# Kernel tuning notes

Hardware: AMD Instinct MI355X
Metric: run time of the kernel (lower is better)

## Reference

```python
import jax, jax.numpy as jnp
import numpy as np

BATCH, STEP, IN_DIM, HID = 16384, 5, 11, 512


def setup_inputs() -> dict:
    key = jax.random.key(0)
    k1, k2, k3, k4, k5 = jax.random.split(key, 5)
    s = 1.0 / np.sqrt(HID)  # torch LSTMCell init scale (uniform +-1/sqrt(hidden))
    return {
        "time_series": jax.random.normal(k1, (BATCH, STEP, IN_DIM), jnp.float32),
        "W_ih": jax.random.uniform(k2, (4 * HID, IN_DIM), jnp.float32, -s, s),
        "W_hh": jax.random.uniform(k3, (4 * HID, HID), jnp.float32, -s, s),
        "b_ih": jax.random.uniform(k4, (4 * HID,), jnp.float32, -s, s),
        "b_hh": jax.random.uniform(k5, (4 * HID,), jnp.float32, -s, s),
    }


def _lstm_scan(time_series, W_ih, W_hh, b_ih, b_hh):
    B = time_series.shape[0]
    H = W_hh.shape[1]
    # Precompute input projections for all steps in one big GEMM: [B, T, 4H]
    x_proj = jnp.einsum('bti,gi->btg', time_series, W_ih) + b_ih + b_hh

    def cell(carry, xg):
        h, c = carry
        gates = xg + h @ W_hh.T  # [B, 4H]
        i, f, g, o = jnp.split(gates, 4, axis=-1)  # torch gate order i,f,g,o
        i = jax.nn.sigmoid(i)
        f = jax.nn.sigmoid(f)
        g = jnp.tanh(g)
        o = jax.nn.sigmoid(o)
        c_new = f * c + i * g
        h_new = o * jnp.tanh(c_new)
        return (h_new, c_new), None

    h0 = jnp.zeros((B, H), time_series.dtype)
    c0 = jnp.zeros((B, H), time_series.dtype)
    (h, c), _ = jax.lax.scan(cell, (h0, c0), jnp.swapaxes(x_proj, 0, 1))
    return c  # original module returns the final cell state c


def reference(time_series, W_ih, W_hh, b_ih, b_hh):
    return _lstm_scan(time_series, W_ih, W_hh, b_ih, b_hh)
```

## Files before the change

### kernel.cpp

```cpp
#include <hip/hip_runtime.h>
#include <hip/hip_bf16.h>


#define HID   512
#define ROWS  64
#define NTHR  1024
#define HBBYTES 36864
#define HB    (HBBYTES / 2)
#define SMEM_HALFS (2 * HB + 64 * 56 + 1024)
#define SMEM_BYTES (SMEM_HALFS * 2)

#define WT_I8   0
#define WT_F16X 1048576
#define WT_CSC  1179648

#define L2E   1.442695041f
#define L2E2  2.885390082f

typedef _Float16 f16x8 __attribute__((ext_vector_type(8)));
typedef float f32x4 __attribute__((ext_vector_type(4)));
typedef int v4i __attribute__((ext_vector_type(4)));

__global__ __launch_bounds__(256) void pack_w(const float* __restrict__ Wih,
                                              const float* __restrict__ Whh,
                                              const float* __restrict__ bih,
                                              const float* __restrict__ bhh,
                                              char* __restrict__ Wt) {
    const int col  = blockIdx.x * 4 + (threadIdx.x >> 6);
    const int lane = threadIdx.x & 63;
    const int g = col >> 9;
    const int j = (col & 511) >> 4;
    const int c = col & 15;

    const float4* __restrict__ src = (const float4*)(Whh + (size_t)col * 512);
    float4 u0 = src[lane * 2 + 0];
    float4 u1 = src[lane * 2 + 1];
    float w[8] = {u0.x, u0.y, u0.z, u0.w, u1.x, u1.y, u1.z, u1.w};

    float m = 0.0f;
#pragma unroll
    for (int q = 0; q < 8; q++) m = fmaxf(m, fabsf(w[q]));
#pragma unroll
    for (int off = 32; off >= 1; off >>= 1)
        m = fmaxf(m, __shfl_xor(m, off));
    m = fmaxf(m, 1e-12f);
    const float inv = 127.0f / m;

    unsigned lo = 0, hi = 0;
#pragma unroll
    for (int q = 0; q < 4; q++)
        lo |= ((unsigned)((int)rintf(w[q] * inv) & 0xff)) << (8 * q);
#pragma unroll
    for (int q = 0; q < 4; q++)
        hi |= ((unsigned)((int)rintf(w[4 + q] * inv) & 0xff)) << (8 * q);

    const int ks8 = lane >> 3;
    const int p   = (lane >> 1) & 3;
    const int bo  = (lane & 1) * 8;
    size_t addr = ((size_t)(j * 8 + ks8) * 4 + g) * 1024 + (c + 16 * p) * 16 + bo;
    uint2 pk = {lo, hi};
    *(uint2*)(Wt + WT_I8 + addr) = pk;

    if (lane == 0) {
        float* csc = (float*)(Wt + WT_CSC);
        csc[col] = (m / 16129.0f) * ((g == 2) ? L2E2 : L2E);
    }

    if (lane < 4) {
        const float scale = (g == 2) ? L2E2 : L2E;
        _Float16 t[8];
        const int kb = lane * 8;
#pragma unroll
        for (int q = 0; q < 8; q++) {
            int k = kb + q;
            float x;
            if (k < 11)       x = Wih[col * 11 + k];
            else if (k == 11) x = bih[col] + bhh[col];
            else              x = 0.0f;
            t[q] = (_Float16)(x * scale);
        }
        *(f16x8*)(Wt + WT_F16X + ((size_t)j * 4 + g) * 1024
                  + (c + 16 * lane) * 16) = *(const f16x8*)t;
    }
}

template <bool FIRST, bool WRITE_H>
__device__ __forceinline__ void run_step(const char* __restrict__ cur,
                                         char* __restrict__ nxt,
                                         const char* __restrict__ wbase,
                                         const float (&sc)[2][4],
                                         f32x4* __restrict__ cacc,
                                         const int wave, const int lane) {
    const int c  = lane & 15;
    const int kq = lane >> 4;
    const int lane16 = lane * 16;
#pragma unroll
    for (int ji = 0; ji < 2; ji++) {
        const int j  = wave * 2 + ji;
        const int jj = __builtin_amdgcn_readfirstlane(j);

        v4i acc[4][4];
        if (!FIRST) {
#pragma unroll
            for (int rt = 0; rt < 4; rt++)
#pragma unroll
                for (int g = 0; g < 4; g++) {
                    v4i z = {0, 0, 0, 0};
                    acc[rt][g] = z;
                }
            const char* __restrict__ w0 = wbase + (size_t)jj * 32768;
            const char* __restrict__ ac = cur + lane16;
#pragma unroll 1
            for (int ks = 0; ks < 8; ks++) {
                v4i B0 = *(const v4i*)(w0 + lane16 + 0);
                v4i B1 = *(const v4i*)(w0 + lane16 + 1024);
                v4i B2 = *(const v4i*)(w0 + lane16 + 2048);
                v4i B3 = *(const v4i*)(w0 + lane16 + 3072);
#pragma unroll
                for (int rt = 0; rt < 4; rt++) {
                    v4i A = *(const v4i*)(ac + rt * 1024);
                    acc[rt][0] = __builtin_amdgcn_mfma_i32_16x16x64_i8(A, B0, acc[rt][0], 0, 0, 0);
                    acc[rt][1] = __builtin_amdgcn_mfma_i32_16x16x64_i8(A, B1, acc[rt][1], 0, 0, 0);
                    acc[rt][2] = __builtin_amdgcn_mfma_i32_16x16x64_i8(A, B2, acc[rt][2], 0, 0, 0);
                    acc[rt][3] = __builtin_amdgcn_mfma_i32_16x16x64_i8(A, B3, acc[rt][3], 0, 0, 0);
                }
                w0 += 4096;
                ac += 4096;
            }
        }

        const char* __restrict__ wx = wbase + WT_F16X + (size_t)jj * 4096;
        f16x8 X0 = *(const f16x8*)(wx + lane16 + 0);
        f16x8 X1 = *(const f16x8*)(wx + lane16 + 1024);
        f16x8 X2 = *(const f16x8*)(wx + lane16 + 2048);
        f16x8 X3 = *(const f16x8*)(wx + lane16 + 3072);
        const char* __restrict__ ax = cur + 32768 + lane16;

#pragma unroll
        for (int rt = 0; rt < 4; rt++) {
            f32x4 g0, g1, g2, g3;
            if (!FIRST) {
#pragma unroll
                for (int r = 0; r < 4; r++) {
                    g0[r] = (float)acc[rt][0][r] * sc[ji][0];
                    g1[r] = (float)acc[rt][1][r] * sc[ji][1];
                    g2[r] = (float)acc[rt][2][r] * sc[ji][2];
                    g3[r] = (float)acc[rt][3][r] * sc[ji][3];
                }
            } else {
                f32x4 z = {0.f, 0.f, 0.f, 0.f};
                g0 = z; g1 = z; g2 = z; g3 = z;
            }
            f16x8 A = *(const f16x8*)(ax + rt * 1024);
            g0 = __builtin_amdgcn_mfma_f32_16x16x32_f16(A, X0, g0, 0, 0, 0);
            g1 = __builtin_amdgcn_mfma_f32_16x16x32_f16(A, X1, g1, 0, 0, 0);
            g2 = __builtin_amdgcn_mfma_f32_16x16x32_f16(A, X2, g2, 0, 0, 0);
            g3 = __builtin_amdgcn_mfma_f32_16x16x32_f16(A, X3, g3, 0, 0, 0);

            f32x4 cv = cacc[ji * 4 + rt];
#pragma unroll
            for (int r = 0; r < 4; r++) {
                float ai = g0[r];
                float af = g1[r];
                float ag = g2[r];
                float ao = g3[r];
                float ei = __builtin_amdgcn_exp2f(-ai);
                float eg = __builtin_amdgcn_exp2f(ag);
                float ig = (eg - 1.0f) *
                           __builtin_amdgcn_rcpf((1.0f + ei) * (1.0f + eg));
                float ef = __builtin_amdgcn_exp2f(-af);
                float cn = __builtin_amdgcn_rcpf(1.0f + ef) * cv[r] + ig;
                cv[r] = cn;
                if (WRITE_H) {
                    float eo = __builtin_amdgcn_exp2f(-ao);
                    float ec = __builtin_amdgcn_exp2f(cn * L2E2);
                    float hn = (ec - 1.0f) *
                               __builtin_amdgcn_rcpf((1.0f + eo) * (1.0f + ec));
                    int q = (int)rintf(hn * 127.0f);
                    nxt[(((j >> 2) * 4 + rt) * 64 + (kq * 4 + r) + 16 * (j & 3)) * 16 + c]
                        = (char)q;
                }
            }
            cacc[ji * 4 + rt] = cv;
        }
    }
}

__device__ __forceinline__ void xfill(_Float16* __restrict__ nxt,
                                      const _Float16* __restrict__ xlds,
                                      int step, int tid) {
    for (int i = tid; i < 64 * 11; i += NTHR) {
        int row = i / 11, xi = i - row * 11;
        int idx = ((32 + (row >> 4)) * 64 + ((row & 15) + 16 * (xi >> 3))) * 8
                  + (xi & 7);
        nxt[idx] = xlds[row * 56 + step * 11 + xi];
    }
}

__global__ __launch_bounds__(NTHR, 4)
void lstm_main(const float* __restrict__ ts,
               const char* __restrict__ Wt,
               float* __restrict__ out) {
    extern __shared__ _Float16 smem[];
    _Float16* buf0h = smem;
    _Float16* buf1h = smem + HB;
    _Float16* xlds  = smem + 2 * HB;
    char* buf0 = (char*)buf0h;
    char* buf1 = (char*)buf1h;
    const int tid  = threadIdx.x;
    const int lane = tid & 63;
    const int wave = tid >> 6;
    const int b0   = blockIdx.x * ROWS;
    const char* wbase = Wt;

    float sc[2][4];
    {
        const float* csc = (const float*)(Wt + WT_CSC);
        const int c = lane & 15;
#pragma unroll
        for (int ji = 0; ji < 2; ji++)
#pragma unroll
            for (int g = 0; g < 4; g++)
                sc[ji][g] = csc[g * 512 + (wave * 2 + ji) * 16 + c];
    }

    {
        f16x8 z = {(_Float16)0, (_Float16)0, (_Float16)0, (_Float16)0,
                   (_Float16)0, (_Float16)0, (_Float16)0, (_Float16)0};
        for (int i = tid * 8; i < 2 * HB; i += NTHR * 8)
            *(f16x8*)(smem + i) = z;
    }
    for (int i = tid; i < 64 * 55; i += NTHR) {
        int row = i / 55, e = i - row * 55;
        xlds[row * 56 + e] = (_Float16)ts[(size_t)(b0 + row) * 55 + e];
    }
    __syncthreads();
    if (tid < 128) {
        int bsel = tid >> 6, row = tid & 63;
        int idx = ((32 + (row >> 4)) * 64 + ((row & 15) + 16)) * 8 + 3;
        (bsel ? buf1h : buf0h)[idx] = (_Float16)1.0f;
    }
    xfill(buf0h, xlds, 0, tid);
    __syncthreads();

    f32x4 cacc[8];
#pragma unroll
    for (int i = 0; i < 8; i++) {
        f32x4 z = {0.f, 0.f, 0.f, 0.f};
        cacc[i] = z;
    }

    run_step<true, true>(buf0, buf1, wbase, sc, cacc, wave, lane);
    xfill(buf1h, xlds, 1, tid);
    __syncthreads();

    for (int t = 1; t < 4; t++) {
        char* cur = (t & 1) ? buf1 : buf0;
        char* nxt = (t & 1) ? buf0 : buf1;
        run_step<false, true>(cur, nxt, wbase, sc, cacc, wave, lane);
        xfill((t & 1) ? (_Float16*)buf0 : (_Float16*)buf1, xlds, t + 1, tid);
        __syncthreads();
    }
    run_step<false, false>(buf0, buf1, wbase, sc, cacc, wave, lane);

    const int c = lane & 15, kq = lane >> 4;
#pragma unroll
    for (int ji = 0; ji < 2; ji++) {
        const int j = wave * 2 + ji;
#pragma unroll
        for (int rt = 0; rt < 4; rt++) {
            f32x4 cv = cacc[ji * 4 + rt];
#pragma unroll
            for (int r = 0; r < 4; r++)
                out[(size_t)(b0 + rt * 16 + kq * 4 + r) * HID + j * 16 + c] = cv[r];
        }
    }
}

extern "C" void kernel_launch(void* const* d_in, const int* in_sizes, int n_in,
                              void* d_out, int out_size, void* d_ws, size_t ws_size,
                              hipStream_t stream) {
    const float* ts  = (const float*)d_in[0];
    const float* Wih = (const float*)d_in[1];
    const float* Whh = (const float*)d_in[2];
    const float* bih = (const float*)d_in[3];
    const float* bhh = (const float*)d_in[4];
    float* out       = (float*)d_out;
    char* Wt         = (char*)d_ws;

    (void)in_sizes; (void)n_in; (void)out_size; (void)ws_size;

    hipFuncSetAttribute(reinterpret_cast<const void*>(lstm_main),
                        hipFuncAttributeMaxDynamicSharedMemorySize, SMEM_BYTES);

    pack_w<<<512, 256, 0, stream>>>(Wih, Whh, bih, bhh, Wt);
    lstm_main<<<256, NTHR, SMEM_BYTES, stream>>>(ts, Wt, out);
}
```

Measured before the change: 213.9 us.

## Halve block threads, give each wave four column tiles with shared A loads

Drops the block to 8 waves. Each wave now owns four hidden-column tiles, handled in two passes of two tiles. In the int8 recurrent GEMM, each A fragment read from LDS now feeds MFMAs for two column tiles instead of one, which halves the A-operand LDS traffic per MFMA. Per-column scales move from registers into an LDS table to save VGPRs. The cost is more accumulators per wave (32 i32x4 plus 16 cell-state vectors), higher register pressure and fewer waves per block to hide latency.

```diff
diff --git a/kernel.cpp b/kernel.cpp
--- a/kernel.cpp
+++ b/kernel.cpp
@@ -4,10 +4,10 @@
 
 #define HID   512
 #define ROWS  64
-#define NTHR  1024
+#define NTHR  512
 #define HBBYTES 36864
 #define HB    (HBBYTES / 2)
-#define SMEM_HALFS (2 * HB + 64 * 56 + 1024)
+#define SMEM_HALFS (2 * HB + 64 * 56 + 4096 + 512)
 #define SMEM_BYTES (SMEM_HALFS * 2)
 
 #define WT_I8   0
@@ -84,80 +84,96 @@
     }
 }
 
-template <bool FIRST, bool WRITE_H>
-__device__ __forceinline__ void run_step(const char* __restrict__ cur,
+template <bool FIRST, int P, bool WRITE_H>
+__device__ __forceinline__ void run_pass(const char* __restrict__ cur,
                                          char* __restrict__ nxt,
                                          const char* __restrict__ wbase,
-                                         const float (&sc)[2][4],
+                                         const float* __restrict__ csc,
                                          f32x4* __restrict__ cacc,
                                          const int wave, const int lane) {
     const int c  = lane & 15;
     const int kq = lane >> 4;
     const int lane16 = lane * 16;
-#pragma unroll
-    for (int ji = 0; ji < 2; ji++) {
-        const int j  = wave * 2 + ji;
-        const int jj = __builtin_amdgcn_readfirstlane(j);
-
-        v4i acc[4][4];
-        if (!FIRST) {
+    const int jj0 = __builtin_amdgcn_readfirstlane(wave * 4 + P * 2);
+
+    v4i acc[2][4][4];
+    if (!FIRST) {
+#pragma unroll
+        for (int ji = 0; ji < 2; ji++)
 #pragma unroll
             for (int rt = 0; rt < 4; rt++)
 #pragma unroll
                 for (int g = 0; g < 4; g++) {
                     v4i z = {0, 0, 0, 0};
-                    acc[rt][g] = z;
+                    acc[ji][rt][g] = z;
                 }
-            const char* __restrict__ w0 = wbase + (size_t)jj * 32768;
-            const char* __restrict__ ac = cur + lane16;
+        const char* __restrict__ w0 = wbase + (size_t)jj0 * 32768;
+        const char* __restrict__ w1 = w0 + 32768;
+        const char* __restrict__ ac = cur + lane16;
 #pragma unroll 1
-            for (int ks = 0; ks < 8; ks++) {
-                v4i B0 = *(const v4i*)(w0 + lane16 + 0);
-                v4i B1 = *(const v4i*)(w0 + lane16 + 1024);
-                v4i B2 = *(const v4i*)(w0 + lane16 + 2048);
-                v4i B3 = *(const v4i*)(w0 + lane16 + 3072);
-#pragma unroll
-                for (int rt = 0; rt < 4; rt++) {
-                    v4i A = *(const v4i*)(ac + rt * 1024);
-                    acc[rt][0] = __builtin_amdgcn_mfma_i32_16x16x64_i8(A, B0, acc[rt][0], 0, 0, 0);
-                    acc[rt][1] = __builtin_amdgcn_mfma_i32_16x16x64_i8(A, B1, acc[rt][1], 0, 0, 0);
-                    acc[rt][2] = __builtin_amdgcn_mfma_i32_16x16x64_i8(A, B2, acc[rt][2], 0, 0, 0);
-                    acc[rt][3] = __builtin_amdgcn_mfma_i32_16x16x64_i8(A, B3, acc[rt][3], 0, 0, 0);
-                }
-                w0 += 4096;
-                ac += 4096;
+        for (int ks = 0; ks < 8; ks++) {
+            v4i B00 = *(const v4i*)(w0 + lane16 + 0);
+            v4i B01 = *(const v4i*)(w0 + lane16 + 1024);
+            v4i B02 = *(const v4i*)(w0 + lane16 + 2048);
+            v4i B03 = *(const v4i*)(w0 + lane16 + 3072);
+            v4i B10 = *(const v4i*)(w1 + lane16 + 0);
+            v4i B11 = *(const v4i*)(w1 + lane16 + 1024);
+            v4i B12 = *(const v4i*)(w1 + lane16 + 2048);
+            v4i B13 = *(const v4i*)(w1 + lane16 + 3072);
+#pragma unroll
+            for (int rt = 0; rt < 4; rt++) {
+                v4i A = *(const v4i*)(ac + rt * 1024);
+                acc[0][rt][0] = __builtin_amdgcn_mfma_i32_16x16x64_i8(A, B00, acc[0][rt][0], 0, 0, 0);
+                acc[0][rt][1] = __builtin_amdgcn_mfma_i32_16x16x64_i8(A, B01, acc[0][rt][1], 0, 0, 0);
+                acc[0][rt][2] = __builtin_amdgcn_mfma_i32_16x16x64_i8(A, B02, acc[0][rt][2], 0, 0, 0);
+                acc[0][rt][3] = __builtin_amdgcn_mfma_i32_16x16x64_i8(A, B03, acc[0][rt][3], 0, 0, 0);
+                acc[1][rt][0] = __builtin_amdgcn_mfma_i32_16x16x64_i8(A, B10, acc[1][rt][0], 0, 0, 0);
+                acc[1][rt][1] = __builtin_amdgcn_mfma_i32_16x16x64_i8(A, B11, acc[1][rt][1], 0, 0, 0);
+                acc[1][rt][2] = __builtin_amdgcn_mfma_i32_16x16x64_i8(A, B12, acc[1][rt][2], 0, 0, 0);
+                acc[1][rt][3] = __builtin_amdgcn_mfma_i32_16x16x64_i8(A, B13, acc[1][rt][3], 0, 0, 0);
             }
+            w0 += 4096;
+            w1 += 4096;
+            ac += 4096;
         }
-
-        const char* __restrict__ wx = wbase + WT_F16X + (size_t)jj * 4096;
-        f16x8 X0 = *(const f16x8*)(wx + lane16 + 0);
-        f16x8 X1 = *(const f16x8*)(wx + lane16 + 1024);
-        f16x8 X2 = *(const f16x8*)(wx + lane16 + 2048);
-        f16x8 X3 = *(const f16x8*)(wx + lane16 + 3072);
-        const char* __restrict__ ax = cur + 32768 + lane16;
-
+    }
+
+    const char* __restrict__ axp = cur + 32768 + lane16;
+#pragma unroll
+    for (int ji = 0; ji < 2; ji++) {
+        const int j  = wave * 4 + P * 2 + ji;
+        const int jj = jj0 + ji;
+        float s0 = csc[0 * 512 + jj * 16 + c];
+        float s1 = csc[1 * 512 + jj * 16 + c];
+        float s2 = csc[2 * 512 + jj * 16 + c];
+        float s3 = csc[3 * 512 + jj * 16 + c];
+        const char* __restrict__ wxj = wbase + WT_F16X + (size_t)jj * 4096;
+        f16x8 X0 = *(const f16x8*)(wxj + lane16 + 0);
+        f16x8 X1 = *(const f16x8*)(wxj + lane16 + 1024);
+        f16x8 X2 = *(const f16x8*)(wxj + lane16 + 2048);
+        f16x8 X3 = *(const f16x8*)(wxj + lane16 + 3072);
 #pragma unroll
         for (int rt = 0; rt < 4; rt++) {
             f32x4 g0, g1, g2, g3;
             if (!FIRST) {
 #pragma unroll
                 for (int r = 0; r < 4; r++) {
-                    g0[r] = (float)acc[rt][0][r] * sc[ji][0];
-                    g1[r] = (float)acc[rt][1][r] * sc[ji][1];
-                    g2[r] = (float)acc[rt][2][r] * sc[ji][2];
-                    g3[r] = (float)acc[rt][3][r] * sc[ji][3];
+                    g0[r] = (float)acc[ji][rt][0][r] * s0;
+                    g1[r] = (float)acc[ji][rt][1][r] * s1;
+                    g2[r] = (float)acc[ji][rt][2][r] * s2;
+                    g3[r] = (float)acc[ji][rt][3][r] * s3;
                 }
             } else {
                 f32x4 z = {0.f, 0.f, 0.f, 0.f};
                 g0 = z; g1 = z; g2 = z; g3 = z;
             }
-            f16x8 A = *(const f16x8*)(ax + rt * 1024);
+            f16x8 A = *(const f16x8*)(axp + rt * 1024);
             g0 = __builtin_amdgcn_mfma_f32_16x16x32_f16(A, X0, g0, 0, 0, 0);
             g1 = __builtin_amdgcn_mfma_f32_16x16x32_f16(A, X1, g1, 0, 0, 0);
             g2 = __builtin_amdgcn_mfma_f32_16x16x32_f16(A, X2, g2, 0, 0, 0);
             g3 = __builtin_amdgcn_mfma_f32_16x16x32_f16(A, X3, g3, 0, 0, 0);
 
-            f32x4 cv = cacc[ji * 4 + rt];
+            f32x4 cv = cacc[(P * 2 + ji) * 4 + rt];
 #pragma unroll
             for (int r = 0; r < 4; r++) {
                 float ai = g0[r];
@@ -181,9 +197,20 @@
                         = (char)q;
                 }
             }
-            cacc[ji * 4 + rt] = cv;
+            cacc[(P * 2 + ji) * 4 + rt] = cv;
         }
     }
+}
+
+template <bool FIRST, bool WRITE_H>
+__device__ __forceinline__ void run_step(const char* __restrict__ cur,
+                                         char* __restrict__ nxt,
+                                         const char* __restrict__ wbase,
+                                         const float* __restrict__ csc,
+                                         f32x4* __restrict__ cacc,
+                                         const int wave, const int lane) {
+    run_pass<FIRST, 0, WRITE_H>(cur, nxt, wbase, csc, cacc, wave, lane);
+    run_pass<FIRST, 1, WRITE_H>(cur, nxt, wbase, csc, cacc, wave, lane);
 }
 
 __device__ __forceinline__ void xfill(_Float16* __restrict__ nxt,
@@ -197,7 +224,7 @@
     }
 }
 
-__global__ __launch_bounds__(NTHR, 4)
+__global__ __launch_bounds__(NTHR, 2)
 void lstm_main(const float* __restrict__ ts,
                const char* __restrict__ Wt,
                float* __restrict__ out) {
@@ -205,6 +232,7 @@
     _Float16* buf0h = smem;
     _Float16* buf1h = smem + HB;
     _Float16* xlds  = smem + 2 * HB;
+    float*    cslds = (float*)(smem + 2 * HB + 64 * 56);
     char* buf0 = (char*)buf0h;
     char* buf1 = (char*)buf1h;
     const int tid  = threadIdx.x;
@@ -213,17 +241,6 @@
     const int b0   = blockIdx.x * ROWS;
     const char* wbase = Wt;
 
-    float sc[2][4];
-    {
-        const float* csc = (const float*)(Wt + WT_CSC);
-        const int c = lane & 15;
-#pragma unroll
-        for (int ji = 0; ji < 2; ji++)
-#pragma unroll
-            for (int g = 0; g < 4; g++)
-                sc[ji][g] = csc[g * 512 + (wave * 2 + ji) * 16 + c];
-    }
-
     {
         f16x8 z = {(_Float16)0, (_Float16)0, (_Float16)0, (_Float16)0,
                    (_Float16)0, (_Float16)0, (_Float16)0, (_Float16)0};
@@ -234,6 +251,8 @@
         int row = i / 55, e = i - row * 55;
         xlds[row * 56 + e] = (_Float16)ts[(size_t)(b0 + row) * 55 + e];
     }
+    for (int i = tid; i < 2048; i += NTHR)
+        cslds[i] = ((const float*)(Wt + WT_CSC))[i];
     __syncthreads();
     if (tid < 128) {
         int bsel = tid >> 6, row = tid & 63;
@@ -243,33 +262,33 @@
     xfill(buf0h, xlds, 0, tid);
     __syncthreads();
 
-    f32x4 cacc[8];
-#pragma unroll
-    for (int i = 0; i < 8; i++) {
+    f32x4 cacc[16];
+#pragma unroll
+    for (int i = 0; i < 16; i++) {
         f32x4 z = {0.f, 0.f, 0.f, 0.f};
         cacc[i] = z;
     }
 
-    run_step<true, true>(buf0, buf1, wbase, sc, cacc, wave, lane);
+    run_step<true, true>(buf0, buf1, wbase, cslds, cacc, wave, lane);
     xfill(buf1h, xlds, 1, tid);
     __syncthreads();
 
     for (int t = 1; t < 4; t++) {
         char* cur = (t & 1) ? buf1 : buf0;
         char* nxt = (t & 1) ? buf0 : buf1;
-        run_step<false, true>(cur, nxt, wbase, sc, cacc, wave, lane);
+        run_step<false, true>(cur, nxt, wbase, cslds, cacc, wave, lane);
         xfill((t & 1) ? (_Float16*)buf0 : (_Float16*)buf1, xlds, t + 1, tid);
         __syncthreads();
     }
-    run_step<false, false>(buf0, buf1, wbase, sc, cacc, wave, lane);
+    run_step<false, false>(buf0, buf1, wbase, cslds, cacc, wave, lane);
 
     const int c = lane & 15, kq = lane >> 4;
 #pragma unroll
-    for (int ji = 0; ji < 2; ji++) {
-        const int j = wave * 2 + ji;
+    for (int jl = 0; jl < 4; jl++) {
+        const int j = wave * 4 + jl;
 #pragma unroll
         for (int rt = 0; rt < 4; rt++) {
-            f32x4 cv = cacc[ji * 4 + rt];
+            f32x4 cv = cacc[jl * 4 + rt];
 #pragma unroll
             for (int r = 0; r < 4; r++)
                 out[(size_t)(b0 + rt * 16 + kq * 4 + r) * HID + j * 16 + c] = cv[r];
```

Result: no change. 215.0 us (+0.5%).
